# Performance work log

Hardware: AMD Instinct MI355X
Metric: run time of the kernel (lower is better)

Reference implementation:

```python
import jax, jax.numpy as jnp
import numpy as np

N_NODES = 100000
N_EDGES = 1600000
NUM_RELS = 16
NUM_BASES = 8
IN_FEATS = 128
N_HIDDEN = 128
N_CLASSES = 40


def _make_layer_params(key, d_in, d_out):
    k0, k1, k2 = jax.random.split(key, 3)
    s_in = 1.0 / np.sqrt(d_in)
    bases = jax.random.normal(k0, (NUM_BASES, d_in, d_out), jnp.float32) * s_in
    comp = jax.random.normal(k1, (NUM_RELS, NUM_BASES), jnp.float32) * (1.0 / np.sqrt(NUM_BASES))
    root = jax.random.normal(k2, (d_in, d_out), jnp.float32) * s_in
    bias = jnp.zeros((d_out,), jnp.float32)
    return bases, comp, root, bias


def setup_inputs() -> dict:
    key = jax.random.key(0)
    ks = jax.random.split(key, 8)
    x = jax.random.normal(ks[0], (N_NODES, IN_FEATS), jnp.float32)
    edge_src = jax.random.randint(ks[1], (N_EDGES,), 0, N_NODES, dtype=jnp.int32)
    edge_dst = jax.random.randint(ks[2], (N_EDGES,), 0, N_NODES, dtype=jnp.int32)
    edge_type = jax.random.randint(ks[3], (N_EDGES,), 0, NUM_RELS, dtype=jnp.int32)
    bases0, comp0, root0, bias0 = _make_layer_params(ks[4], IN_FEATS, N_HIDDEN)
    bases1, comp1, root1, bias1 = _make_layer_params(ks[5], N_HIDDEN, N_HIDDEN)
    bases2, comp2, root2, bias2 = _make_layer_params(ks[6], N_HIDDEN, N_CLASSES)
    return dict(x=x, edge_src=edge_src, edge_dst=edge_dst, edge_type=edge_type,
                bases0=bases0, comp0=comp0, root0=root0, bias0=bias0,
                bases1=bases1, comp1=comp1, root1=root1, bias1=bias1,
                bases2=bases2, comp2=comp2, root2=root2, bias2=bias2)


def _rgcn_layer(x, edge_src, edge_dst, edge_type, bases, comp, root, bias):
    # basis decomposition: W_r = sum_b comp[r,b] * bases[b]   -> [R, d_in, d_out]
    W = jnp.einsum('rb,bio->rio', comp, bases)
    # transform all node features under every relation (R small, dense GEMMs)
    xw = jnp.einsum('ni,rio->rno', x, W)                    # [R, N, d_out]
    # per-edge message: gather by (relation, source) -- irregular access
    msg = xw[edge_type, edge_src]                           # [E, d_out]
    # mean aggregation per (destination, relation), as in PyG RGCNConv (aggr='mean')
    seg = edge_dst * NUM_RELS + edge_type                   # [E]
    deg = jax.ops.segment_sum(jnp.ones((msg.shape[0],), x.dtype), seg,
                              num_segments=N_NODES * NUM_RELS)
    norm = 1.0 / jnp.maximum(deg[seg], 1.0)                 # [E]
    agg = jax.ops.segment_sum(msg * norm[:, None], edge_dst, num_segments=N_NODES)
    return agg + x @ root + bias


def reference(x, edge_src, edge_dst, edge_type,
              bases0, comp0, root0, bias0,
              bases1, comp1, root1, bias1,
              bases2, comp2, root2, bias2):
    # dropout is identity at inference; activation='relu' on all but last layer
    h = _rgcn_layer(x, edge_src, edge_dst, edge_type, bases0, comp0, root0, bias0)
    h = jax.nn.relu(h)
    h = _rgcn_layer(h, edge_src, edge_dst, edge_type, bases1, comp1, root1, bias1)
    h = jax.nn.relu(h)
    h = _rgcn_layer(h, edge_src, edge_dst, edge_type, bases2, comp2, root2, bias2)
    return h
```

## Files before the change

kernel.cpp:

```cpp
#include <hip/hip_runtime.h>
#include <hip/hip_bf16.h>

#define NNODES 100000
#define NEDGES 1600000
#define NRELS 16
#define NBASES 8
#define DFEAT 128
#define NCLS 40
#define MAXDEG 64
#define KTOT 1152

typedef __attribute__((ext_vector_type(8))) short bf16x8v;
typedef __attribute__((ext_vector_type(4))) float f32x4v;
typedef __attribute__((ext_vector_type(2))) float f32x2v;

struct __align__(8) bf16x4s { __hip_bfloat162 lo, hi; };

__global__ __launch_bounds__(256)
void k_cvq(const float* __restrict__ x, __hip_bfloat16* __restrict__ xb,
           short* __restrict__ q8, float* __restrict__ qs, int nrows)
{
    int wave = threadIdx.x >> 6, lane = threadIdx.x & 63;
    int v = blockIdx.x * 4 + wave;
    if (v >= nrows) return;
    float2 xv = ((const float2*)x)[(size_t)v * 64 + lane];
    __hip_bfloat162 bv;
    bv.x = __float2bfloat16(xv.x);
    bv.y = __float2bfloat16(xv.y);
    ((__hip_bfloat162*)xb)[(size_t)v * 64 + lane] = bv;
    float m = fmaxf(fabsf(xv.x), fabsf(xv.y));
#pragma unroll
    for (int o = 32; o; o >>= 1) m = fmaxf(m, __shfl_xor(m, o));
    float inv = (m > 0.f) ? 127.f / m : 0.f;
    int qx = (int)rintf(xv.x * inv), qy = (int)rintf(xv.y * inv);
    q8[(size_t)v * 64 + lane] = (short)((qx & 0xff) | (qy << 8));
    if (lane == 0) qs[v] = m * (1.f / 127.f);
}

__global__ __launch_bounds__(256)
void k_build(const int* __restrict__ esrc, const int* __restrict__ edst,
             const int* __restrict__ etyp,
             unsigned* __restrict__ degD, unsigned* __restrict__ ell)
{
    int e = blockIdx.x * 256 + threadIdx.x;
    if (e >= NEDGES) return;
    int d = edst[e], t = etyp[e], s = esrc[e];
    unsigned slot = atomicAdd(&degD[d], 1u);
    if (slot < MAXDEG) ell[(size_t)d * MAXDEG + slot] = ((unsigned)s << 4) | (unsigned)t;
}

__global__ __launch_bounds__(256)
void k_quant(const __hip_bfloat16* __restrict__ h,
             short* __restrict__ q8, float* __restrict__ qs, int nrows)
{
    int wave = threadIdx.x >> 6, lane = threadIdx.x & 63;
    int v = blockIdx.x * 4 + wave;
    if (v >= nrows) return;
    __hip_bfloat162 xv = ((const __hip_bfloat162*)h)[(size_t)v * 64 + lane];
    float xl = __bfloat162float(xv.x), xh = __bfloat162float(xv.y);
    float m = fmaxf(fabsf(xl), fabsf(xh));
#pragma unroll
    for (int o = 32; o; o >>= 1) m = fmaxf(m, __shfl_xor(m, o));
    float inv = (m > 0.f) ? 127.f / m : 0.f;
    int qx = (int)rintf(xl * inv), qy = (int)rintf(xh * inv);
    q8[(size_t)v * 64 + lane] = (short)((qx & 0xff) | (qy << 8));
    if (lane == 0) qs[v] = m * (1.f / 127.f);
}

__global__ __launch_bounds__(256)
void k_agg(const short* __restrict__ q8, const float* __restrict__ qs,
           const __hip_bfloat16* __restrict__ hin,
           const unsigned* __restrict__ ell,
           const unsigned* __restrict__ degD,
           const float* __restrict__ comp,
           __hip_bfloat16* __restrict__ A,
           int r0, int rows)
{
    __shared__ float compS[NRELS * NBASES];
    __shared__ __align__(16) float cS[8][MAXDEG][8];
    __shared__ unsigned sS[8][MAXDEG];
    __shared__ unsigned histS[8][NRELS];
    if (threadIdx.x < NRELS * NBASES) compS[threadIdx.x] = comp[threadIdx.x];
    __syncthreads();

    int wave = threadIdx.x >> 6, lane = threadIdx.x & 63;
    int half = lane >> 5, hl = lane & 31;
    int node = wave * 2 + half;
    int rl = blockIdx.x * 8 + node;
    bool alive = (rl < rows);
    int v = alive ? (r0 + rl) : 0;
    int ne = alive ? (int)degD[v] : 0; if (ne > MAXDEG) ne = MAXDEG;

    if (alive) {
        const unsigned* erow = ell + (size_t)v * MAXDEG;
        unsigned p0 = (hl < ne) ? erow[hl] : 0u;
        unsigned p1 = (hl + 32 < ne) ? erow[hl + 32] : 0u;
        if (hl < NRELS) histS[node][hl] = 0u;
        if (hl < ne)      atomicAdd(&histS[node][p0 & 15u], 1u);
        if (hl + 32 < ne) atomicAdd(&histS[node][p1 & 15u], 1u);
#pragma unroll
        for (int r = 0; r < 2; r++) {
            unsigned p = r ? p1 : p0;
            int slot = hl + 32 * r;
            bool val = (slot < ne);
            unsigned t = p & 15u;
            int s = val ? (int)(p >> 4) : 0;
            unsigned cnt = val ? histS[node][t] : 1u;
            if (cnt < 1u) cnt = 1u;
            float w = val ? (qs[s] / (float)cnt) : 0.f;
            f32x4v c0, c1;
#pragma unroll
            for (int b = 0; b < 4; b++) c0[b] = compS[t * NBASES + b] * w;
#pragma unroll
            for (int b = 0; b < 4; b++) c1[b] = compS[t * NBASES + 4 + b] * w;
            *(f32x4v*)&cS[node][slot][0] = c0;
            *(f32x4v*)&cS[node][slot][4] = c1;
            sS[node][slot] = (unsigned)s;
        }
    }

    f32x2v accA[NBASES], accB[NBASES];
#pragma unroll
    for (int b = 0; b < NBASES; b++) { accA[b] = (f32x2v){0.f,0.f}; accB[b] = (f32x2v){0.f,0.f}; }

    if (alive) {
        for (int e0 = 0; e0 < ne; e0 += 16) {
            unsigned qd[16];
#pragma unroll
            for (int j = 0; j < 16; j++) {
                unsigned s = sS[node][e0 + j];
                qd[j] = ((const unsigned*)(q8 + (size_t)s * 64))[hl];
            }
#pragma unroll
            for (int j = 0; j < 16; j++) {
                f32x4v ca = *(const f32x4v*)&cS[node][e0 + j][0];
                f32x4v cb = *(const f32x4v*)&cS[node][e0 + j][4];
                unsigned d = qd[j];
                f32x2v f01, f23;
                f01.x = (float)(char)(d & 0xff);
                f01.y = (float)(char)((d >> 8) & 0xff);
                f23.x = (float)(char)((d >> 16) & 0xff);
                f23.y = (float)(char)(d >> 24);
                accA[0] += ca[0] * f01;  accB[0] += ca[0] * f23;
                accA[1] += ca[1] * f01;  accB[1] += ca[1] * f23;
                accA[2] += ca[2] * f01;  accB[2] += ca[2] * f23;
                accA[3] += ca[3] * f01;  accB[3] += ca[3] * f23;
                accA[4] += cb[0] * f01;  accB[4] += cb[0] * f23;
                accA[5] += cb[1] * f01;  accB[5] += cb[1] * f23;
                accA[6] += cb[2] * f01;  accB[6] += cb[2] * f23;
                accA[7] += cb[3] * f01;  accB[7] += cb[3] * f23;
            }
        }
        __hip_bfloat16* Arow = A + (size_t)rl * KTOT;
#pragma unroll
        for (int b = 0; b < NBASES; b++) {
            bf16x4s o;
            o.lo.x = __float2bfloat16(accA[b].x);
            o.lo.y = __float2bfloat16(accA[b].y);
            o.hi.x = __float2bfloat16(accB[b].x);
            o.hi.y = __float2bfloat16(accB[b].y);
            *(bf16x4s*)&Arow[b * 128 + 4 * hl] = o;
        }
        *(bf16x4s*)&Arow[1024 + 4 * hl] =
            *(const bf16x4s*)&hin[(size_t)v * 128 + 4 * hl];
    }
}

__global__ __launch_bounds__(256)
void k_w(const float* __restrict__ bases, const float* __restrict__ root,
         __hip_bfloat16* __restrict__ WT, int dout, int npad)
{
    int idx = blockIdx.x * 256 + threadIdx.x;
    int total = npad * KTOT;
    if (idx >= total) return;
    int o = idx / KTOT, k = idx - o * KTOT;
    float v = 0.f;
    if (o < dout) v = (k < 1024) ? bases[k * dout + o] : root[(k - 1024) * dout + o];
    WT[idx] = __float2bfloat16(v);
}

template<int NT, bool RELU, bool FINAL>
__global__ __launch_bounds__(256)
void k_gemm(const __hip_bfloat16* __restrict__ A,
            const __hip_bfloat16* __restrict__ WT,
            const float* __restrict__ bias,
            void* __restrict__ outp,
            int r0, int rows, int dout)
{
    constexpr int WM = (NT == 128) ? 2 : 4;
    constexpr int WN = 4 / WM;
    constexpr int MT = 128 / (16 * WM);
    constexpr int NTW = NT / (16 * WN);
    __shared__ __align__(16) __hip_bfloat16 As[128 * 32];
    __shared__ __align__(16) __hip_bfloat16 Bs[NT * 32];
    int tid = threadIdx.x;
    int wave = tid >> 6, lane = tid & 63;
    int wm = wave % WM, wn = wave / WM;
    int bm = blockIdx.x * 128;
    int lm = lane & 15, lq = lane >> 4;
    f32x4v zero = {0.f, 0.f, 0.f, 0.f};
    f32x4v acc[MT][NTW];
#pragma unroll
    for (int a = 0; a < MT; a++)
#pragma unroll
        for (int b = 0; b < NTW; b++) acc[a][b] = zero;

    for (int k0 = 0; k0 < KTOT; k0 += 32) {
#pragma unroll
        for (int j = 0; j < 2; j++) {
            int slot = tid + 256 * j;
            int row = slot >> 2, kc = (slot & 3) << 3;
            __builtin_amdgcn_global_load_lds(
                (const __attribute__((address_space(1))) void*)
                    &A[(size_t)(bm + row) * KTOT + k0 + kc],
                (__attribute__((address_space(3))) void*)&As[slot * 8],
                16, 0, 0);
        }
#pragma unroll
        for (int j = 0; j < NT / 64; j++) {
            int slot = tid + 256 * j;
            int row = slot >> 2, kc = (slot & 3) << 3;
            __builtin_amdgcn_global_load_lds(
                (const __attribute__((address_space(1))) void*)
                    &WT[(size_t)row * KTOT + k0 + kc],
                (__attribute__((address_space(3))) void*)&Bs[slot * 8],
                16, 0, 0);
        }
        __syncthreads();
        bf16x8v af[MT], bfr[NTW];
#pragma unroll
        for (int mt = 0; mt < MT; mt++)
            af[mt] = *(const bf16x8v*)&As[(wm * (16 * MT) + mt * 16 + lm) * 32 + lq * 8];
#pragma unroll
        for (int nt = 0; nt < NTW; nt++)
            bfr[nt] = *(const bf16x8v*)&Bs[(wn * (16 * NTW) + nt * 16 + lm) * 32 + lq * 8];
#pragma unroll
        for (int mt = 0; mt < MT; mt++)
#pragma unroll
            for (int nt = 0; nt < NTW; nt++)
                acc[mt][nt] = __builtin_amdgcn_mfma_f32_16x16x32_bf16(
                    af[mt], bfr[nt], acc[mt][nt], 0, 0, 0);
        __syncthreads();
    }
#pragma unroll
    for (int mt = 0; mt < MT; mt++) {
        int rbase = bm + wm * (16 * MT) + mt * 16 + lq * 4;
#pragma unroll
        for (int nt = 0; nt < NTW; nt++) {
            int col = wn * (16 * NTW) + nt * 16 + lm;
#pragma unroll
            for (int i = 0; i < 4; i++) {
                int rl = rbase + i;
                if (rl < rows && col < dout) {
                    float v = acc[mt][nt][i] + bias[col];
                    if (RELU) v = fmaxf(v, 0.f);
                    if (FINAL)
                        ((float*)outp)[(size_t)(r0 + rl) * NCLS + col] = v;
                    else
                        ((__hip_bfloat16*)outp)[(size_t)(r0 + rl) * DFEAT + col] =
                            __float2bfloat16(v);
                }
            }
        }
    }
}

extern "C" void kernel_launch(void* const* d_in, const int* in_sizes, int n_in,
                              void* d_out, int out_size, void* d_ws, size_t ws_size,
                              hipStream_t stream)
{
    const float* x  = (const float*)d_in[0];
    const int* esrc = (const int*)d_in[1];
    const int* edst = (const int*)d_in[2];
    const int* etyp = (const int*)d_in[3];
    const float* basesA[3] = {(const float*)d_in[4], (const float*)d_in[8], (const float*)d_in[12]};
    const float* compA[3]  = {(const float*)d_in[5], (const float*)d_in[9], (const float*)d_in[13]};
    const float* rootA[3]  = {(const float*)d_in[6], (const float*)d_in[10], (const float*)d_in[14]};
    const float* biasA[3]  = {(const float*)d_in[7], (const float*)d_in[11], (const float*)d_in[15]};

    size_t off = 0;
    char* base = (char*)d_ws;
    auto carve = [&](size_t bytes) -> void* {
        void* r = base + off;
        off += (bytes + 255) & ~(size_t)255;
        return r;
    };
    __hip_bfloat16* xb = (__hip_bfloat16*)carve((size_t)NNODES * DFEAT * 2);
    __hip_bfloat16* h1 = (__hip_bfloat16*)carve((size_t)NNODES * DFEAT * 2);
    __hip_bfloat16* WT = (__hip_bfloat16*)carve((size_t)128 * KTOT * 2);
    unsigned* ell  = (unsigned*)carve((size_t)NNODES * MAXDEG * 4);
    unsigned* degD = (unsigned*)carve((size_t)NNODES * 4);
    short* q8  = (short*)carve((size_t)NNODES * 64 * 2);
    float* qsc = (float*)carve((size_t)NNODES * 4);
    __hip_bfloat16* h2 = xb;

    if (ws_size <= off) return;
    size_t arows = (ws_size - off) / ((size_t)KTOT * 2);
    if (arows > 100096) arows = 100096;
    int chunk = (int)(arows & ~(size_t)127);
    if (chunk < 128) return;
    __hip_bfloat16* A = (__hip_bfloat16*)(base + off);

    hipMemsetAsync(degD, 0, (size_t)NNODES * 4, stream);
    k_cvq<<<(NNODES + 3) / 4, 256, 0, stream>>>(x, xb, q8, qsc, NNODES);
    k_build<<<(NEDGES + 255) / 256, 256, 0, stream>>>(esrc, edst, etyp, degD, ell);

    const __hip_bfloat16* hin = xb;
    __hip_bfloat16* houts[2] = {h1, h2};
    for (int l = 0; l < 3; l++) {
        int dout = (l == 2) ? NCLS : DFEAT;
        int npad = (l == 2) ? 64 : 128;
        if (l > 0)
            k_quant<<<(NNODES + 3) / 4, 256, 0, stream>>>(hin, q8, qsc, NNODES);
        k_w<<<(npad * KTOT + 255) / 256, 256, 0, stream>>>(basesA[l], rootA[l], WT, dout, npad);
        for (int r0 = 0; r0 < NNODES; r0 += chunk) {
            int rows = NNODES - r0; if (rows > chunk) rows = chunk;
            k_agg<<<(rows + 7) / 8, 256, 0, stream>>>(q8, qsc, hin, ell, degD, compA[l], A, r0, rows);
            int gm = (rows + 127) / 128;
            if (l < 2)
                k_gemm<128, true, false><<<gm, 256, 0, stream>>>(A, WT, biasA[l], houts[l], r0, rows, dout);
            else
                k_gemm<64, false, true><<<gm, 256, 0, stream>>>(A, WT, biasA[l], d_out, r0, rows, dout);
        }
        if (l < 2) hin = houts[l];
    }
}
```

Measured before the change: 778.8 us.

## Bin edges by destination before ELL build; read root features directly in GEMM

The ELL build now runs in two passes. Edges are first binned into 16 destination-range buckets, then scattered per bucket, so the degree atomics and ELL writes hit a localized region and get better cache locality. The aggregation kernel no longer copies the node's own bf16 features into the concatenated A matrix. Instead the GEMM runs a second K loop that reads hin and a separate root weight matrix directly, which shrinks A and removes one write and one read of 128 columns per row. The bins buffer aliases the A workspace and requires extra workspace capacity. The GEMM may read hin rows past NNODES on the last tile, since the bounds are not guarded.

```diff
diff --git a/kernel.cpp b/kernel.cpp
--- a/kernel.cpp
+++ b/kernel.cpp
@@ -8,7 +8,12 @@
 #define DFEAT 128
 #define NCLS 40
 #define MAXDEG 64
-#define KTOT 1152
+#define KG 1024
+#define KR 128
+#define NBUCK 16
+#define BSHIFT 13
+#define BCAP 163840
+#define BPB 160
 
 typedef __attribute__((ext_vector_type(8))) short bf16x8v;
 typedef __attribute__((ext_vector_type(4))) float f32x4v;
@@ -38,15 +43,53 @@
 }
 
 __global__ __launch_bounds__(256)
-void k_build(const int* __restrict__ esrc, const int* __restrict__ edst,
-             const int* __restrict__ etyp,
-             unsigned* __restrict__ degD, unsigned* __restrict__ ell)
-{
-    int e = blockIdx.x * 256 + threadIdx.x;
-    if (e >= NEDGES) return;
-    int d = edst[e], t = etyp[e], s = esrc[e];
-    unsigned slot = atomicAdd(&degD[d], 1u);
-    if (slot < MAXDEG) ell[(size_t)d * MAXDEG + slot] = ((unsigned)s << 4) | (unsigned)t;
+void k_bin(const int* __restrict__ esrc, const int* __restrict__ edst,
+           const int* __restrict__ etyp,
+           uint2* __restrict__ bins, unsigned* __restrict__ gcount)
+{
+    __shared__ unsigned hist[NBUCK], gbase[NBUCK];
+    int tid = threadIdx.x;
+    if (tid < NBUCK) hist[tid] = 0u;
+    __syncthreads();
+    int e = blockIdx.x * 256 + tid;
+    bool val = (e < NEDGES);
+    int b = 0; unsigned rank = 0; uint2 rec = {0u, 0u};
+    if (val) {
+        int d = edst[e];
+        b = d >> BSHIFT;
+        rec.x = ((unsigned)esrc[e] << 4) | (unsigned)etyp[e];
+        rec.y = (unsigned)d;
+        rank = atomicAdd(&hist[b], 1u);
+    }
+    __syncthreads();
+    if (tid < NBUCK) gbase[tid] = atomicAdd(&gcount[tid], hist[tid]);
+    __syncthreads();
+    if (val) {
+        unsigned pos = gbase[b] + rank;
+        if (pos < BCAP) bins[(size_t)b * BCAP + pos] = rec;
+    }
+}
+
+__global__ __launch_bounds__(256)
+void k_scat(const uint2* __restrict__ bins, const unsigned* __restrict__ gcount,
+            unsigned* __restrict__ degD, unsigned* __restrict__ ell)
+{
+    int bkt = blockIdx.x / BPB;
+    int blk = blockIdx.x % BPB;
+    unsigned cnt = gcount[bkt];
+    if (cnt > BCAP) cnt = BCAP;
+    unsigned base = (unsigned)blk * 1024u;
+    if (base >= cnt) return;
+    const uint2* bp = bins + (size_t)bkt * BCAP;
+#pragma unroll
+    for (int i = 0; i < 4; i++) {
+        unsigned idx = base + i * 256 + threadIdx.x;
+        if (idx < cnt) {
+            uint2 r = bp[idx];
+            unsigned slot = atomicAdd(&degD[r.y], 1u);
+            if (slot < MAXDEG) ell[(size_t)r.y * MAXDEG + slot] = r.x;
+        }
+    }
 }
 
 __global__ __launch_bounds__(256)
@@ -69,7 +112,6 @@
 
 __global__ __launch_bounds__(256)
 void k_agg(const short* __restrict__ q8, const float* __restrict__ qs,
-           const __hip_bfloat16* __restrict__ hin,
            const unsigned* __restrict__ ell,
            const unsigned* __restrict__ degD,
            const float* __restrict__ comp,
@@ -102,12 +144,12 @@
         for (int r = 0; r < 2; r++) {
             unsigned p = r ? p1 : p0;
             int slot = hl + 32 * r;
-            bool val = (slot < ne);
+            bool vl = (slot < ne);
             unsigned t = p & 15u;
-            int s = val ? (int)(p >> 4) : 0;
-            unsigned cnt = val ? histS[node][t] : 1u;
+            int s = vl ? (int)(p >> 4) : 0;
+            unsigned cnt = vl ? histS[node][t] : 1u;
             if (cnt < 1u) cnt = 1u;
-            float w = val ? (qs[s] / (float)cnt) : 0.f;
+            float w = vl ? (qs[s] / (float)cnt) : 0.f;
             f32x4v c0, c1;
 #pragma unroll
             for (int b = 0; b < 4; b++) c0[b] = compS[t * NBASES + b] * w;
@@ -151,7 +193,7 @@
                 accA[7] += cb[3] * f01;  accB[7] += cb[3] * f23;
             }
         }
-        __hip_bfloat16* Arow = A + (size_t)rl * KTOT;
+        __hip_bfloat16* Arow = A + (size_t)rl * KG;
 #pragma unroll
         for (int b = 0; b < NBASES; b++) {
             bf16x4s o;
@@ -161,28 +203,31 @@
             o.hi.y = __float2bfloat16(accB[b].y);
             *(bf16x4s*)&Arow[b * 128 + 4 * hl] = o;
         }
-        *(bf16x4s*)&Arow[1024 + 4 * hl] =
-            *(const bf16x4s*)&hin[(size_t)v * 128 + 4 * hl];
     }
 }
 
 __global__ __launch_bounds__(256)
 void k_w(const float* __restrict__ bases, const float* __restrict__ root,
-         __hip_bfloat16* __restrict__ WT, int dout, int npad)
+         __hip_bfloat16* __restrict__ WTb, __hip_bfloat16* __restrict__ WTr,
+         int dout, int npad)
 {
     int idx = blockIdx.x * 256 + threadIdx.x;
-    int total = npad * KTOT;
+    int total = npad * (KG + KR);
     if (idx >= total) return;
-    int o = idx / KTOT, k = idx - o * KTOT;
+    int o = idx / (KG + KR), k = idx - o * (KG + KR);
     float v = 0.f;
-    if (o < dout) v = (k < 1024) ? bases[k * dout + o] : root[(k - 1024) * dout + o];
-    WT[idx] = __float2bfloat16(v);
+    if (o < dout) v = (k < KG) ? bases[(size_t)k * dout + o]
+                               : root[(size_t)(k - KG) * dout + o];
+    if (k < KG) WTb[(size_t)o * KG + k] = __float2bfloat16(v);
+    else        WTr[(size_t)o * KR + (k - KG)] = __float2bfloat16(v);
 }
 
 template<int NT, bool RELU, bool FINAL>
 __global__ __launch_bounds__(256)
 void k_gemm(const __hip_bfloat16* __restrict__ A,
-            const __hip_bfloat16* __restrict__ WT,
+            const __hip_bfloat16* __restrict__ WTb,
+            const __hip_bfloat16* __restrict__ hin,
+            const __hip_bfloat16* __restrict__ WTr,
             const float* __restrict__ bias,
             void* __restrict__ outp,
             int r0, int rows, int dout)
@@ -198,21 +243,20 @@
     int wm = wave % WM, wn = wave / WM;
     int bm = blockIdx.x * 128;
     int lm = lane & 15, lq = lane >> 4;
-    f32x4v zero = {0.f, 0.f, 0.f, 0.f};
     f32x4v acc[MT][NTW];
 #pragma unroll
     for (int a = 0; a < MT; a++)
 #pragma unroll
-        for (int b = 0; b < NTW; b++) acc[a][b] = zero;
-
-    for (int k0 = 0; k0 < KTOT; k0 += 32) {
+        for (int b = 0; b < NTW; b++) acc[a][b] = (f32x4v){0.f,0.f,0.f,0.f};
+
+    for (int k0 = 0; k0 < KG; k0 += 32) {
 #pragma unroll
         for (int j = 0; j < 2; j++) {
             int slot = tid + 256 * j;
             int row = slot >> 2, kc = (slot & 3) << 3;
             __builtin_amdgcn_global_load_lds(
                 (const __attribute__((address_space(1))) void*)
-                    &A[(size_t)(bm + row) * KTOT + k0 + kc],
+                    &A[(size_t)(bm + row) * KG + k0 + kc],
                 (__attribute__((address_space(3))) void*)&As[slot * 8],
                 16, 0, 0);
         }
@@ -222,7 +266,7 @@
             int row = slot >> 2, kc = (slot & 3) << 3;
             __builtin_amdgcn_global_load_lds(
                 (const __attribute__((address_space(1))) void*)
-                    &WT[(size_t)row * KTOT + k0 + kc],
+                    &WTb[(size_t)row * KG + k0 + kc],
                 (__attribute__((address_space(3))) void*)&Bs[slot * 8],
                 16, 0, 0);
         }
@@ -242,17 +286,57 @@
                     af[mt], bfr[nt], acc[mt][nt], 0, 0, 0);
         __syncthreads();
     }
+
+    for (int kk = 0; kk < KR; kk += 32) {
+#pragma unroll
+        for (int j = 0; j < 2; j++) {
+            int slot = tid + 256 * j;
+            int row = slot >> 2, kc = (slot & 3) << 3;
+            __builtin_amdgcn_global_load_lds(
+                (const __attribute__((address_space(1))) void*)
+                    &hin[(size_t)(r0 + bm + row) * KR + kk + kc],
+                (__attribute__((address_space(3))) void*)&As[slot * 8],
+                16, 0, 0);
+        }
+#pragma unroll
+        for (int j = 0; j < NT / 64; j++) {
+            int slot = tid + 256 * j;
+            int row = slot >> 2, kc = (slot & 3) << 3;
+            __builtin_amdgcn_global_load_lds(
+                (const __attribute__((address_space(1))) void*)
+                    &WTr[(size_t)row * KR + kk + kc],
+                (__attribute__((address_space(3))) void*)&Bs[slot * 8],
+                16, 0, 0);
+        }
+        __syncthreads();
+        bf16x8v af[MT], bfr[NTW];
+#pragma unroll
+        for (int mt = 0; mt < MT; mt++)
+            af[mt] = *(const bf16x8v*)&As[(wm * (16 * MT) + mt * 16 + lm) * 32 + lq * 8];
+#pragma unroll
+        for (int nt = 0; nt < NTW; nt++)
+            bfr[nt] = *(const bf16x8v*)&Bs[(wn * (16 * NTW) + nt * 16 + lm) * 32 + lq * 8];
+#pragma unroll
+        for (int mt = 0; mt < MT; mt++)
+#pragma unroll
+            for (int nt = 0; nt < NTW; nt++)
+                acc[mt][nt] = __builtin_amdgcn_mfma_f32_16x16x32_bf16(
+                    af[mt], bfr[nt], acc[mt][nt], 0, 0, 0);
+        __syncthreads();
+    }
+
 #pragma unroll
     for (int mt = 0; mt < MT; mt++) {
         int rbase = bm + wm * (16 * MT) + mt * 16 + lq * 4;
 #pragma unroll
         for (int nt = 0; nt < NTW; nt++) {
             int col = wn * (16 * NTW) + nt * 16 + lm;
+            float bc = bias[col < dout ? col : 0];
 #pragma unroll
             for (int i = 0; i < 4; i++) {
                 int rl = rbase + i;
                 if (rl < rows && col < dout) {
-                    float v = acc[mt][nt][i] + bias[col];
+                    float v = acc[mt][nt][i] + bc;
                     if (RELU) v = fmaxf(v, 0.f);
                     if (FINAL)
                         ((float*)outp)[(size_t)(r0 + rl) * NCLS + col] = v;
@@ -287,23 +371,30 @@
     };
     __hip_bfloat16* xb = (__hip_bfloat16*)carve((size_t)NNODES * DFEAT * 2);
     __hip_bfloat16* h1 = (__hip_bfloat16*)carve((size_t)NNODES * DFEAT * 2);
-    __hip_bfloat16* WT = (__hip_bfloat16*)carve((size_t)128 * KTOT * 2);
-    unsigned* ell  = (unsigned*)carve((size_t)NNODES * MAXDEG * 4);
-    unsigned* degD = (unsigned*)carve((size_t)NNODES * 4);
+    __hip_bfloat16* WTb = (__hip_bfloat16*)carve((size_t)128 * KG * 2);
+    __hip_bfloat16* WTr = (__hip_bfloat16*)carve((size_t)128 * KR * 2);
+    unsigned* ell    = (unsigned*)carve((size_t)NNODES * MAXDEG * 4);
+    unsigned* degD   = (unsigned*)carve((size_t)NNODES * 4);
+    unsigned* gcount = (unsigned*)carve(NBUCK * 4);
     short* q8  = (short*)carve((size_t)NNODES * 64 * 2);
     float* qsc = (float*)carve((size_t)NNODES * 4);
     __hip_bfloat16* h2 = xb;
 
     if (ws_size <= off) return;
-    size_t arows = (ws_size - off) / ((size_t)KTOT * 2);
+    size_t abytes = ws_size - off;
+    uint2* bins = (uint2*)(base + off);
+    if (abytes < (size_t)NBUCK * BCAP * 8) return;
+    size_t arows = abytes / ((size_t)KG * 2);
     if (arows > 100096) arows = 100096;
     int chunk = (int)(arows & ~(size_t)127);
     if (chunk < 128) return;
     __hip_bfloat16* A = (__hip_bfloat16*)(base + off);
 
-    hipMemsetAsync(degD, 0, (size_t)NNODES * 4, stream);
+    (void)hipMemsetAsync(degD, 0, (size_t)NNODES * 4, stream);
+    (void)hipMemsetAsync(gcount, 0, NBUCK * 4, stream);
     k_cvq<<<(NNODES + 3) / 4, 256, 0, stream>>>(x, xb, q8, qsc, NNODES);
-    k_build<<<(NEDGES + 255) / 256, 256, 0, stream>>>(esrc, edst, etyp, degD, ell);
+    k_bin<<<(NEDGES + 255) / 256, 256, 0, stream>>>(esrc, edst, etyp, bins, gcount);
+    k_scat<<<NBUCK * BPB, 256, 0, stream>>>(bins, gcount, degD, ell);
 
     const __hip_bfloat16* hin = xb;
     __hip_bfloat16* houts[2] = {h1, h2};
@@ -312,15 +403,15 @@
         int npad = (l == 2) ? 64 : 128;
         if (l > 0)
             k_quant<<<(NNODES + 3) / 4, 256, 0, stream>>>(hin, q8, qsc, NNODES);
-        k_w<<<(npad * KTOT + 255) / 256, 256, 0, stream>>>(basesA[l], rootA[l], WT, dout, npad);
+        k_w<<<(npad * (KG + KR) + 255) / 256, 256, 0, stream>>>(basesA[l], rootA[l], WTb, WTr, dout, npad);
         for (int r0 = 0; r0 < NNODES; r0 += chunk) {
             int rows = NNODES - r0; if (rows > chunk) rows = chunk;
-            k_agg<<<(rows + 7) / 8, 256, 0, stream>>>(q8, qsc, hin, ell, degD, compA[l], A, r0, rows);
+            k_agg<<<(rows + 7) / 8, 256, 0, stream>>>(q8, qsc, ell, degD, compA[l], A, r0, rows);
             int gm = (rows + 127) / 128;
             if (l < 2)
-                k_gemm<128, true, false><<<gm, 256, 0, stream>>>(A, WT, biasA[l], houts[l], r0, rows, dout);
+                k_gemm<128, true, false><<<gm, 256, 0, stream>>>(A, WTb, hin, WTr, biasA[l], houts[l], r0, rows, dout);
             else
-                k_gemm<64, false, true><<<gm, 256, 0, stream>>>(A, WT, biasA[l], d_out, r0, rows, dout);
+                k_gemm<64, false, true><<<gm, 256, 0, stream>>>(A, WTb, hin, WTr, biasA[l], d_out, r0, rows, dout);
         }
         if (l < 2) hin = houts[l];
     }
```

Result: slower. 843.4 us (+8.3%).
